# Performance work log

Hardware: AMD Instinct MI355X
Metric: run time of the kernel (lower is better)

## Reference

```python
import jax, jax.numpy as jnp
import numpy as np

N_NODES = 2000
N_EDGES = 8000  # undirected; 2*N_EDGES directed pairs
BATCH = 16
D = 64  # in/out node and edge feature dim


def _build_graph():
    """Random undirected graph; returns directed (src, dst) pairs in the
    row-major order of torch.where(adj==1), plus the undirected edge id of
    each directed pair (mimics get_all_edge_for_node_pairs)."""
    rng = np.random.default_rng(0)
    cand = rng.integers(0, N_NODES, size=(6 * N_EDGES, 2))
    cand = cand[cand[:, 0] != cand[:, 1]]
    cand = np.sort(cand, axis=1)
    cand = np.unique(cand, axis=0)
    und = cand[:N_EDGES]  # [E,2] unique undirected edges
    adj = np.zeros((N_NODES, N_NODES), dtype=np.int64)
    eid = np.full((N_NODES, N_NODES), -1, dtype=np.int64)
    e = np.arange(N_EDGES)
    adj[und[:, 0], und[:, 1]] = 1
    adj[und[:, 1], und[:, 0]] = 1
    eid[und[:, 0], und[:, 1]] = e
    eid[und[:, 1], und[:, 0]] = e
    src, dst = np.nonzero(adj)  # row-major, like torch.where
    edge_idx = eid[src, dst]
    return src.astype(np.int32), dst.astype(np.int32), edge_idx.astype(np.int32)


def setup_inputs() -> dict:
    key = jax.random.key(0)
    ks = jax.random.split(key, 7)
    src, dst, eidx = _build_graph()
    s = 0.05
    return {
        "x": jax.random.normal(ks[0], (BATCH, N_EDGES + N_NODES, D), jnp.float32),
        "W_edge": jax.random.normal(ks[1], (D, D), jnp.float32) * s,
        "W_node": jax.random.normal(ks[2], (D, D), jnp.float32) * s,
        "b_node": jax.random.normal(ks[3], (D,), jnp.float32) * s,
        "W_comb": jax.random.normal(ks[4], (3 * D, D), jnp.float32) * s,
        "b_comb": jax.random.normal(ks[5], (D,), jnp.float32) * s,
        "w_attn": jax.random.normal(ks[6], (D, 1), jnp.float32) * s,
        "src": jnp.asarray(src),
        "dst": jnp.asarray(dst),
        "eidx": jnp.asarray(eidx),
        "num_edges": N_EDGES,
    }


def reference(x, W_edge, W_node, b_node, W_comb, b_comb, w_attn, src, dst, eidx, num_edges):
    E = num_edges
    edges = x[:, :E]            # [B,E,D]
    nodes = x[:, E:]            # [B,N,D]
    B, N = nodes.shape[0], nodes.shape[1]
    f = edges @ W_edge          # dense_edge (no bias)      [B,E,D]
    h = nodes @ W_node + b_node  # dense_node (bias)        [B,N,D]
    # gather per directed edge: src node, edge feat, dst node -> [B,2E,3D]
    g = jnp.concatenate([h[:, src], f[:, eidx], h[:, dst]], axis=-1)
    f_out = jax.nn.leaky_relu(g @ W_comb + b_comb, negative_slope=0.01)  # [B,2E,D]
    # attention logits -> softmax over ALL directed edges (dim=1, as in torch)
    alpha = jax.nn.softmax(jnp.einsum('bed,do->beo', f_out, w_attn), axis=1)[..., 0]  # [B,2E]
    # scatter into dense per-batch adjacency, then aggregate
    adj = jnp.zeros((B, N, N), x.dtype).at[:, src, dst].set(alpha)
    h_out = jnp.einsum('bnm,bmd->bnd', adj, h)  # [B,N,D]
    return jnp.concatenate([f_out, h_out], axis=1)  # [B,2E+N,D]
```

## Files before the change

### kernel.cpp

```cpp
#include <hip/hip_runtime.h>
#include <hip/hip_bf16.h>

#define B_ 16
#define N_ 2000
#define E_ 8000
#define P_ 16000
#define XROW (E_ + N_)
#define OROW (P_ + N_)

typedef __hip_bfloat16 bf16;
typedef unsigned short u16;
typedef unsigned int u32;
typedef __attribute__((ext_vector_type(8))) short short8;
typedef __attribute__((ext_vector_type(4))) float f32x4;

__device__ __forceinline__ float b2f(bf16 v) { return __bfloat162float(v); }
__device__ __forceinline__ float u2f(u16 u) { return __uint_as_float(((u32)u) << 16); }
__device__ __forceinline__ float lo2f(u32 u) { return __uint_as_float(u << 16); }
__device__ __forceinline__ float hi2f(u32 u) { return __uint_as_float(u & 0xFFFF0000u); }
__device__ __forceinline__ u16 f2bu(float v) {
  bf16 b = __float2bfloat16(v);
  return *reinterpret_cast<u16*>(&b);
}

__device__ __forceinline__ float ldin(const void* p, int i, int f32) {
  return f32 ? ((const float*)p)[i] : __bfloat162float(((const bf16*)p)[i]);
}

__device__ __forceinline__ int detect_f32(const void* x) {
  int lane = threadIdx.x & 63;
  ushort4 v = reinterpret_cast<const ushort4*>(x)[lane];
  int bad = 0;
  float f0 = u2f(v.x), f1 = u2f(v.y), f2 = u2f(v.z), f3 = u2f(v.w);
  if (!(fabsf(f0) < 1e4f)) bad++;
  if (!(fabsf(f1) < 1e4f)) bad++;
  if (!(fabsf(f2) < 1e4f)) bad++;
  if (!(fabsf(f3) < 1e4f)) bad++;
  unsigned long long m = __ballot(bad > 0);
  return __popcll(m) > 8;
}

__device__ __forceinline__ ushort4 ld4b(const void* p, size_t i, int f32) {
  ushort4 o;
  if (f32) {
    float4 v = *reinterpret_cast<const float4*>((const float*)p + i);
    o.x = f2bu(v.x); o.y = f2bu(v.y); o.z = f2bu(v.z); o.w = f2bu(v.w);
  } else {
    o = *reinterpret_cast<const ushort4*>((const u16*)p + i);
  }
  return o;
}

__global__ __launch_bounds__(256) void k_pre(
    const void* __restrict__ x,
    const void* __restrict__ W_edge, const void* __restrict__ W_node,
    const void* __restrict__ b_node, const void* __restrict__ W_comb,
    float* __restrict__ A1, float* __restrict__ A2, float* __restrict__ A3,
    float* __restrict__ c1, float* __restrict__ c3) {
  const int f32 = detect_f32(x);
  int o = blockIdx.x * 256 + threadIdx.x;
  if (o < 4096) {
    int i = o >> 6, j = o & 63;
    float a = 0.f;
    for (int k = 0; k < 64; ++k) a += ldin(W_node, i*64+k, f32) * ldin(W_comb, k*64+j, f32);
    A1[o] = a;
  } else if (o < 8192) {
    int oo = o - 4096; int i = oo >> 6, j = oo & 63;
    float a = 0.f;
    for (int k = 0; k < 64; ++k) a += ldin(W_edge, i*64+k, f32) * ldin(W_comb, (64+k)*64+j, f32);
    A2[oo] = a;
  } else if (o < 12288) {
    int oo = o - 8192; int i = oo >> 6, j = oo & 63;
    float a = 0.f;
    for (int k = 0; k < 64; ++k) a += ldin(W_node, i*64+k, f32) * ldin(W_comb, (128+k)*64+j, f32);
    A3[oo] = a;
  } else if (o < 12352) {
    int j = o - 12288;
    float a = 0.f;
    for (int k = 0; k < 64; ++k) a += ldin(b_node, k, f32) * ldin(W_comb, k*64+j, f32);
    c1[j] = a;
  } else if (o < 12416) {
    int j = o - 12352;
    float a = 0.f;
    for (int k = 0; k < 64; ++k) a += ldin(b_node, k, f32) * ldin(W_comb, (128+k)*64+j, f32);
    c3[j] = a;
  }
}

#define PITCH 72
__global__ __launch_bounds__(256) void k_transform(
    const void* __restrict__ x, const void* __restrict__ W_node,
    const void* __restrict__ b_node,
    const float* __restrict__ A1, const float* __restrict__ A2,
    const float* __restrict__ A3,
    const float* __restrict__ c1, const float* __restrict__ c3,
    bf16* __restrict__ h, bf16* __restrict__ hs, bf16* __restrict__ hd,
    bf16* __restrict__ fe) {
  __shared__ u16 smem[128*PITCH + 64*PITCH < 256*PITCH ? 256*PITCH : 256*PITCH];
  const int f32 = detect_f32(x);
  int t = threadIdx.x;
  int wave = t >> 6, lane = t & 63;
  int m16 = lane & 15, q = lane >> 4;
  if (blockIdx.x < 500) {
    u16* xs = smem;
    u16* Wt = smem + 64*PITCH;
    int row0 = blockIdx.x * 64;
    for (int i = t*4; i < 4096; i += 1024) {
      int r = i >> 6, k = i & 63;
      int row = row0 + r;
      int b = row / N_, n = row - b * N_;
      *reinterpret_cast<ushort4*>(&xs[r*PITCH + k]) =
          ld4b(x, (size_t)(b * XROW + E_ + n) * 64 + k, f32);
    }
    for (int idx = t; idx < 192*16; idx += 256) {
      int c = idx >> 4, kg = (idx & 15) * 4;
      ushort4 o;
      u16* ov = (u16*)&o;
      #pragma unroll
      for (int j = 0; j < 4; ++j) {
        int k = kg + j;
        float v;
        if (c < 64)        v = ldin(W_node, k*64 + c, f32);
        else if (c < 128)  v = A1[k*64 + (c - 64)];
        else               v = A3[k*64 + (c - 128)];
        ov[j] = f2bu(v);
      }
      *reinterpret_cast<ushort4*>(&Wt[c*PITCH + kg]) = o;
    }
    __syncthreads();
    int mrow = wave*16 + m16;
    short8 af0 = *reinterpret_cast<short8*>(&xs[mrow*PITCH + q*8]);
    short8 af1 = *reinterpret_cast<short8*>(&xs[mrow*PITCH + 32 + q*8]);
    f32x4 acc[12];
    #pragma unroll
    for (int c = 0; c < 12; ++c) acc[c] = (f32x4){0.f, 0.f, 0.f, 0.f};
    #pragma unroll
    for (int c = 0; c < 12; ++c) {
      short8 bf0 = *reinterpret_cast<short8*>(&Wt[(c*16 + m16)*PITCH + q*8]);
      short8 bf1 = *reinterpret_cast<short8*>(&Wt[(c*16 + m16)*PITCH + 32 + q*8]);
      acc[c] = __builtin_amdgcn_mfma_f32_16x16x32_bf16(af0, bf0, acc[c], 0, 0, 0);
      acc[c] = __builtin_amdgcn_mfma_f32_16x16x32_bf16(af1, bf1, acc[c], 0, 0, 0);
    }
    #pragma unroll
    for (int c = 0; c < 12; ++c) {
      int seg = c >> 2;
      int lcol = (c*16 + m16) & 63;
      float bias = (seg == 0) ? ldin(b_node, lcol, f32) : (seg == 1 ? c1[lcol] : c3[lcol]);
      bf16* tgt = (seg == 0) ? h : (seg == 1 ? hs : hd);
      #pragma unroll
      for (int r = 0; r < 4; ++r) {
        int row = row0 + wave*16 + q*4 + r;
        tgt[(size_t)row*64 + lcol] = __float2bfloat16(acc[c][r] + bias);
      }
    }
  } else {
    u16* xs = smem;
    u16* Wt = smem + 128*PITCH;
    int row0 = (blockIdx.x - 500) * 128;
    for (int i = t*4; i < 8192; i += 1024) {
      int r = i >> 6, k = i & 63;
      int row = row0 + r;
      int b = row / E_, e = row - b * E_;
      *reinterpret_cast<ushort4*>(&xs[r*PITCH + k]) =
          ld4b(x, (size_t)(b * XROW + e) * 64 + k, f32);
    }
    for (int idx = t; idx < 64*16; idx += 256) {
      int c = idx >> 4, kg = (idx & 15) * 4;
      ushort4 o;
      u16* ov = (u16*)&o;
      #pragma unroll
      for (int j = 0; j < 4; ++j) ov[j] = f2bu(A2[(kg + j)*64 + c]);
      *reinterpret_cast<ushort4*>(&Wt[c*PITCH + kg]) = o;
    }
    __syncthreads();
    short8 af[2][2];
    #pragma unroll
    for (int rt = 0; rt < 2; ++rt) {
      int mrow = wave*32 + rt*16 + m16;
      af[rt][0] = *reinterpret_cast<short8*>(&xs[mrow*PITCH + q*8]);
      af[rt][1] = *reinterpret_cast<short8*>(&xs[mrow*PITCH + 32 + q*8]);
    }
    f32x4 acc[2][4];
    #pragma unroll
    for (int rt = 0; rt < 2; ++rt)
      #pragma unroll
      for (int c = 0; c < 4; ++c) acc[rt][c] = (f32x4){0.f, 0.f, 0.f, 0.f};
    #pragma unroll
    for (int c = 0; c < 4; ++c) {
      short8 bf0 = *reinterpret_cast<short8*>(&Wt[(c*16 + m16)*PITCH + q*8]);
      short8 bf1 = *reinterpret_cast<short8*>(&Wt[(c*16 + m16)*PITCH + 32 + q*8]);
      #pragma unroll
      for (int rt = 0; rt < 2; ++rt) {
        acc[rt][c] = __builtin_amdgcn_mfma_f32_16x16x32_bf16(af[rt][0], bf0, acc[rt][c], 0, 0, 0);
        acc[rt][c] = __builtin_amdgcn_mfma_f32_16x16x32_bf16(af[rt][1], bf1, acc[rt][c], 0, 0, 0);
      }
    }
    #pragma unroll
    for (int rt = 0; rt < 2; ++rt)
      #pragma unroll
      for (int c = 0; c < 4; ++c) {
        int col = c*16 + m16;
        #pragma unroll
        for (int r = 0; r < 4; ++r) {
          int row = row0 + wave*32 + rt*16 + q*4 + r;
          fe[(size_t)row*64 + col] = __float2bfloat16(acc[rt][c][r]);
        }
      }
  }
}

__global__ __launch_bounds__(256) void k_combine(
    const void* __restrict__ x,
    const bf16* __restrict__ hs, const bf16* __restrict__ hd,
    const bf16* __restrict__ fe, const void* __restrict__ b_comb,
    const void* __restrict__ w_attn,
    const int* __restrict__ src, const int* __restrict__ dst,
    const int* __restrict__ eidx,
    void* __restrict__ out, float* __restrict__ logits,
    float* __restrict__ mpart, float* __restrict__ spart) {
  const int f32 = detect_f32(x);
  __shared__ float bias[64], watt[64];
  __shared__ float ld_log[32];
  int t = threadIdx.x;
  if (t < 64) { bias[t] = ldin(b_comb, t, f32); watt[t] = ldin(w_attn, t, f32); }
  __syncthreads();
  int lane = t & 63, wave = t >> 6;
  int grp = lane >> 3, sub = lane & 7, c0 = sub * 8;
  int r = blockIdx.x * 32 + wave * 8 + grp;
  int b = r / P_, p = r - b * P_;
  int s = src[p], d2 = dst[p], e = eidx[p];
  uint4 ua = *reinterpret_cast<const uint4*>((const u16*)hs + (size_t)(b*N_ + s)*64 + c0);
  uint4 uf = *reinterpret_cast<const uint4*>((const u16*)fe + (size_t)(b*E_ + e)*64 + c0);
  uint4 ud = *reinterpret_cast<const uint4*>((const u16*)hd + (size_t)(b*N_ + d2)*64 + c0);
  float v[8];
  v[0] = lo2f(ua.x) + lo2f(uf.x) + lo2f(ud.x) + bias[c0+0];
  v[1] = hi2f(ua.x) + hi2f(uf.x) + hi2f(ud.x) + bias[c0+1];
  v[2] = lo2f(ua.y) + lo2f(uf.y) + lo2f(ud.y) + bias[c0+2];
  v[3] = hi2f(ua.y) + hi2f(uf.y) + hi2f(ud.y) + bias[c0+3];
  v[4] = lo2f(ua.z) + lo2f(uf.z) + lo2f(ud.z) + bias[c0+4];
  v[5] = hi2f(ua.z) + hi2f(uf.z) + hi2f(ud.z) + bias[c0+5];
  v[6] = lo2f(ua.w) + lo2f(uf.w) + lo2f(ud.w) + bias[c0+6];
  v[7] = hi2f(ua.w) + hi2f(uf.w) + hi2f(ud.w) + bias[c0+7];
  float l = 0.f;
  #pragma unroll
  for (int j = 0; j < 8; ++j) {
    v[j] = v[j] > 0.f ? v[j] : 0.01f * v[j];
    l += v[j] * watt[c0 + j];
  }
  size_t obase = (size_t)(b*OROW + p)*64 + c0;
  if (f32) {
    float4 o0; o0.x = v[0]; o0.y = v[1]; o0.z = v[2]; o0.w = v[3];
    float4 o1; o1.x = v[4]; o1.y = v[5]; o1.z = v[6]; o1.w = v[7];
    *reinterpret_cast<float4*>((float*)out + obase)     = o0;
    *reinterpret_cast<float4*>((float*)out + obase + 4) = o1;
  } else {
    uint4 o;
    o.x = ((u32)f2bu(v[1]) << 16) | f2bu(v[0]);
    o.y = ((u32)f2bu(v[3]) << 16) | f2bu(v[2]);
    o.z = ((u32)f2bu(v[5]) << 16) | f2bu(v[4]);
    o.w = ((u32)f2bu(v[7]) << 16) | f2bu(v[6]);
    *reinterpret_cast<uint4*>((u16*)out + obase) = o;
  }
  l += __shfl_down(l, 4, 8);
  l += __shfl_down(l, 2, 8);
  l += __shfl_down(l, 1, 8);
  if (sub == 0) {
    logits[b*P_ + p] = l;
    ld_log[wave * 8 + grp] = l;
  }
  __syncthreads();
  if (t < 32) {
    float li = ld_log[t];
    float m = li;
    #pragma unroll
    for (int o = 16; o > 0; o >>= 1) m = fmaxf(m, __shfl_xor(m, o, 32));
    float sv = __expf(li - m);
    #pragma unroll
    for (int o = 16; o > 0; o >>= 1) sv += __shfl_xor(sv, o, 32);
    if (t == 0) { mpart[blockIdx.x] = m; spart[blockIdx.x] = sv; }
  }
}

__global__ __launch_bounds__(256) void k_hout(
    const void* __restrict__ x,
    const bf16* __restrict__ h, const float* __restrict__ logits,
    const float* __restrict__ mpart, const float* __restrict__ spart,
    const int* __restrict__ src, const int* __restrict__ dst,
    void* __restrict__ out) {
  const int f32 = detect_f32(x);
  int n = blockIdx.x;
  int t = threadIdx.x;
  int wave = t >> 6, lane = t & 63;
  int b = blockIdx.y * 4 + wave;
  float m = -1e30f, s = 0.f;
  for (int j = lane; j < 500; j += 64) {
    float mj = mpart[500*b + j], sj = spart[500*b + j];
    float nm = fmaxf(m, mj);
    s = s * __expf(m - nm) + sj * __expf(mj - nm);
    m = nm;
  }
  #pragma unroll
  for (int o = 32; o > 0; o >>= 1) {
    float mo = __shfl_xor(m, o, 64);
    float so = __shfl_xor(s, o, 64);
    float nm = fmaxf(m, mo);
    s = s * __expf(m - nm) + so * __expf(mo - nm);
    m = nm;
  }
  float inv = 1.0f / s;
  int lo = 0, hi = P_;
  while (lo < hi) { int mid = (lo + hi) >> 1; if (src[mid] < n) lo = mid + 1; else hi = mid; }
  int start = lo;
  hi = P_;
  while (lo < hi) { int mid = (lo + hi) >> 1; if (src[mid] <= n) lo = mid + 1; else hi = mid; }
  int end = lo;
  int grp = lane >> 4, sub = lane & 15, c0 = sub * 4;
  float a0 = 0.f, a1 = 0.f, a2 = 0.f, a3 = 0.f;
  for (int p = start + grp; p < end; p += 4) {
    float a = __expf(logits[b*P_ + p] - m) * inv;
    int dn = dst[p];
    ushort4 hv = *reinterpret_cast<const ushort4*>((const u16*)h + (size_t)(b*N_ + dn)*64 + c0);
    a0 += a * u2f(hv.x); a1 += a * u2f(hv.y);
    a2 += a * u2f(hv.z); a3 += a * u2f(hv.w);
  }
  a0 += __shfl_xor(a0, 16, 64); a0 += __shfl_xor(a0, 32, 64);
  a1 += __shfl_xor(a1, 16, 64); a1 += __shfl_xor(a1, 32, 64);
  a2 += __shfl_xor(a2, 16, 64); a2 += __shfl_xor(a2, 32, 64);
  a3 += __shfl_xor(a3, 16, 64); a3 += __shfl_xor(a3, 32, 64);
  if (grp == 0) {
    size_t obase = (size_t)(b*OROW + P_ + n)*64 + c0;
    if (f32) {
      float4 o4; o4.x = a0; o4.y = a1; o4.z = a2; o4.w = a3;
      *reinterpret_cast<float4*>((float*)out + obase) = o4;
    } else {
      ushort4 o4;
      o4.x = f2bu(a0); o4.y = f2bu(a1); o4.z = f2bu(a2); o4.w = f2bu(a3);
      *reinterpret_cast<ushort4*>((u16*)out + obase) = o4;
    }
  }
}

extern "C" void kernel_launch(void* const* d_in, const int* in_sizes, int n_in,
                              void* d_out, int out_size, void* d_ws, size_t ws_size,
                              hipStream_t stream) {
  const void* x      = d_in[0];
  const void* W_edge = d_in[1];
  const void* W_node = d_in[2];
  const void* b_node = d_in[3];
  const void* W_comb = d_in[4];
  const void* b_comb = d_in[5];
  const void* w_attn = d_in[6];
  const int* src  = (const int*)d_in[7];
  const int* dst  = (const int*)d_in[8];
  const int* eidx = (const int*)d_in[9];

  float* A1 = (float*)d_ws;
  float* A2 = A1 + 4096;
  float* A3 = A2 + 4096;
  float* c1 = A3 + 4096;
  float* c3 = c1 + 64;
  float* logits = c3 + 64;
  float* mpart = logits + B_*P_;
  float* spart = mpart + 8000;
  bf16* h  = (bf16*)(spart + 8000);
  bf16* hs = h  + B_*N_*64;
  bf16* hd = hs + B_*N_*64;
  bf16* fe = hd + B_*N_*64;

  k_pre<<<49, 256, 0, stream>>>(x, W_edge, W_node, b_node, W_comb, A1, A2, A3, c1, c3);
  k_transform<<<1500, 256, 0, stream>>>(x, W_node, b_node, A1, A2, A3, c1, c3, h, hs, hd, fe);
  k_combine<<<(B_*P_)/32, 256, 0, stream>>>(x, hs, hd, fe, b_comb, w_attn, src, dst, eidx, d_out, logits, mpart, spart);
  k_hout<<<dim3(N_, B_/4), 256, 0, stream>>>(x, h, logits, mpart, spart, src, dst, d_out);
}
```

Measured before the change: 196.4 us.

## Precompute bf16 transposed weights, CSR rowptr, and softmax stats in separate kernels

k_pre now writes the transposed bf16 combined weight matrices and a CSR row pointer for src, so k_transform no longer rebuilds weight tiles in shared memory per block. k_transform loads MFMA operands straight from global memory without LDS staging. A new k_smerge kernel merges the per-block softmax max/sum once per batch, and k_hout reads those values plus rowptr instead of redoing the reduction and binary searches in every block. This adds one kernel launch and relies on uncoalesced global fragment loads in the transform.

```diff
diff --git a/kernel.cpp b/kernel.cpp
--- a/kernel.cpp
+++ b/kernel.cpp
@@ -40,106 +40,95 @@
   return __popcll(m) > 8;
 }
 
-__device__ __forceinline__ ushort4 ld4b(const void* p, size_t i, int f32) {
-  ushort4 o;
+__device__ __forceinline__ short8 ld8b(const void* p, size_t i, int f32) {
+  short8 r;
   if (f32) {
-    float4 v = *reinterpret_cast<const float4*>((const float*)p + i);
-    o.x = f2bu(v.x); o.y = f2bu(v.y); o.z = f2bu(v.z); o.w = f2bu(v.w);
+    const float* f = (const float*)p + i;
+    float4 v0 = *reinterpret_cast<const float4*>(f);
+    float4 v1 = *reinterpret_cast<const float4*>(f + 4);
+    u16* o = (u16*)&r;
+    o[0] = f2bu(v0.x); o[1] = f2bu(v0.y); o[2] = f2bu(v0.z); o[3] = f2bu(v0.w);
+    o[4] = f2bu(v1.x); o[5] = f2bu(v1.y); o[6] = f2bu(v1.z); o[7] = f2bu(v1.w);
   } else {
-    o = *reinterpret_cast<const ushort4*>((const u16*)p + i);
-  }
-  return o;
+    r = *reinterpret_cast<const short8*>((const u16*)p + i);
+  }
+  return r;
 }
 
 __global__ __launch_bounds__(256) void k_pre(
     const void* __restrict__ x,
     const void* __restrict__ W_edge, const void* __restrict__ W_node,
     const void* __restrict__ b_node, const void* __restrict__ W_comb,
-    float* __restrict__ A1, float* __restrict__ A2, float* __restrict__ A3,
-    float* __restrict__ c1, float* __restrict__ c3) {
+    const int* __restrict__ src,
+    u16* __restrict__ Wtn, u16* __restrict__ Wte,
+    float* __restrict__ c1, float* __restrict__ c3,
+    int* __restrict__ rowptr) {
   const int f32 = detect_f32(x);
   int o = blockIdx.x * 256 + threadIdx.x;
   if (o < 4096) {
-    int i = o >> 6, j = o & 63;
+    int c = o >> 6, k = o & 63;
+    Wtn[c*64 + k] = f2bu(ldin(W_node, k*64 + c, f32));
+  } else if (o < 12288) {
+    int oo = o - 4096;
+    int cc = oo >> 6, k = oo & 63;
+    int col = cc & 63;
+    int base = (cc < 64) ? 0 : 128;
     float a = 0.f;
-    for (int k = 0; k < 64; ++k) a += ldin(W_node, i*64+k, f32) * ldin(W_comb, k*64+j, f32);
-    A1[o] = a;
-  } else if (o < 8192) {
-    int oo = o - 4096; int i = oo >> 6, j = oo & 63;
+    for (int j = 0; j < 64; ++j)
+      a += ldin(W_node, k*64 + j, f32) * ldin(W_comb, (base + j)*64 + col, f32);
+    Wtn[(64 + cc)*64 + k] = f2bu(a);
+  } else if (o < 16384) {
+    int oo = o - 12288;
+    int c = oo >> 6, k = oo & 63;
     float a = 0.f;
-    for (int k = 0; k < 64; ++k) a += ldin(W_edge, i*64+k, f32) * ldin(W_comb, (64+k)*64+j, f32);
-    A2[oo] = a;
-  } else if (o < 12288) {
-    int oo = o - 8192; int i = oo >> 6, j = oo & 63;
+    for (int j = 0; j < 64; ++j)
+      a += ldin(W_edge, k*64 + j, f32) * ldin(W_comb, (64 + j)*64 + c, f32);
+    Wte[c*64 + k] = f2bu(a);
+  } else if (o < 16448) {
+    int j = o - 16384;
     float a = 0.f;
-    for (int k = 0; k < 64; ++k) a += ldin(W_node, i*64+k, f32) * ldin(W_comb, (128+k)*64+j, f32);
-    A3[oo] = a;
-  } else if (o < 12352) {
-    int j = o - 12288;
+    for (int k = 0; k < 64; ++k) a += ldin(b_node, k, f32) * ldin(W_comb, k*64 + j, f32);
+    c1[j] = a;
+  } else if (o < 16512) {
+    int j = o - 16448;
     float a = 0.f;
-    for (int k = 0; k < 64; ++k) a += ldin(b_node, k, f32) * ldin(W_comb, k*64+j, f32);
-    c1[j] = a;
-  } else if (o < 12416) {
-    int j = o - 12352;
-    float a = 0.f;
-    for (int k = 0; k < 64; ++k) a += ldin(b_node, k, f32) * ldin(W_comb, (128+k)*64+j, f32);
+    for (int k = 0; k < 64; ++k) a += ldin(b_node, k, f32) * ldin(W_comb, (128 + k)*64 + j, f32);
     c3[j] = a;
-  }
-}
-
-#define PITCH 72
+  } else if (o < 16512 + N_ + 1) {
+    int n = o - 16512;
+    int lo = 0, hi = P_;
+    while (lo < hi) { int mid = (lo + hi) >> 1; if (src[mid] < n) lo = mid + 1; else hi = mid; }
+    rowptr[n] = lo;
+  }
+}
+
 __global__ __launch_bounds__(256) void k_transform(
-    const void* __restrict__ x, const void* __restrict__ W_node,
+    const void* __restrict__ x,
+    const u16* __restrict__ Wtn, const u16* __restrict__ Wte,
     const void* __restrict__ b_node,
-    const float* __restrict__ A1, const float* __restrict__ A2,
-    const float* __restrict__ A3,
     const float* __restrict__ c1, const float* __restrict__ c3,
     bf16* __restrict__ h, bf16* __restrict__ hs, bf16* __restrict__ hd,
     bf16* __restrict__ fe) {
-  __shared__ u16 smem[128*PITCH + 64*PITCH < 256*PITCH ? 256*PITCH : 256*PITCH];
   const int f32 = detect_f32(x);
   int t = threadIdx.x;
   int wave = t >> 6, lane = t & 63;
   int m16 = lane & 15, q = lane >> 4;
   if (blockIdx.x < 500) {
-    u16* xs = smem;
-    u16* Wt = smem + 64*PITCH;
-    int row0 = blockIdx.x * 64;
-    for (int i = t*4; i < 4096; i += 1024) {
-      int r = i >> 6, k = i & 63;
-      int row = row0 + r;
-      int b = row / N_, n = row - b * N_;
-      *reinterpret_cast<ushort4*>(&xs[r*PITCH + k]) =
-          ld4b(x, (size_t)(b * XROW + E_ + n) * 64 + k, f32);
-    }
-    for (int idx = t; idx < 192*16; idx += 256) {
-      int c = idx >> 4, kg = (idx & 15) * 4;
-      ushort4 o;
-      u16* ov = (u16*)&o;
-      #pragma unroll
-      for (int j = 0; j < 4; ++j) {
-        int k = kg + j;
-        float v;
-        if (c < 64)        v = ldin(W_node, k*64 + c, f32);
-        else if (c < 128)  v = A1[k*64 + (c - 64)];
-        else               v = A3[k*64 + (c - 128)];
-        ov[j] = f2bu(v);
-      }
-      *reinterpret_cast<ushort4*>(&Wt[c*PITCH + kg]) = o;
-    }
-    __syncthreads();
-    int mrow = wave*16 + m16;
-    short8 af0 = *reinterpret_cast<short8*>(&xs[mrow*PITCH + q*8]);
-    short8 af1 = *reinterpret_cast<short8*>(&xs[mrow*PITCH + 32 + q*8]);
+    int row0 = blockIdx.x * 64 + wave * 16;
+    int arow = row0 + m16;
+    int b = arow / N_, n = arow - b * N_;
+    size_t xbase = (size_t)(b * XROW + E_ + n) * 64;
+    short8 af0 = ld8b(x, xbase + q*8, f32);
+    short8 af1 = ld8b(x, xbase + 32 + q*8, f32);
     f32x4 acc[12];
     #pragma unroll
     for (int c = 0; c < 12; ++c) acc[c] = (f32x4){0.f, 0.f, 0.f, 0.f};
     #pragma unroll
     for (int c = 0; c < 12; ++c) {
-      short8 bf0 = *reinterpret_cast<short8*>(&Wt[(c*16 + m16)*PITCH + q*8]);
-      short8 bf1 = *reinterpret_cast<short8*>(&Wt[(c*16 + m16)*PITCH + 32 + q*8]);
-      acc[c] = __builtin_amdgcn_mfma_f32_16x16x32_bf16(af0, bf0, acc[c], 0, 0, 0);
-      acc[c] = __builtin_amdgcn_mfma_f32_16x16x32_bf16(af1, bf1, acc[c], 0, 0, 0);
+      short8 b0 = *reinterpret_cast<const short8*>(&Wtn[(c*16 + m16)*64 + q*8]);
+      short8 b1 = *reinterpret_cast<const short8*>(&Wtn[(c*16 + m16)*64 + 32 + q*8]);
+      acc[c] = __builtin_amdgcn_mfma_f32_16x16x32_bf16(af0, b0, acc[c], 0, 0, 0);
+      acc[c] = __builtin_amdgcn_mfma_f32_16x16x32_bf16(af1, b1, acc[c], 0, 0, 0);
     }
     #pragma unroll
     for (int c = 0; c < 12; ++c) {
@@ -149,36 +138,20 @@
       bf16* tgt = (seg == 0) ? h : (seg == 1 ? hs : hd);
       #pragma unroll
       for (int r = 0; r < 4; ++r) {
-        int row = row0 + wave*16 + q*4 + r;
+        int row = row0 + q*4 + r;
         tgt[(size_t)row*64 + lcol] = __float2bfloat16(acc[c][r] + bias);
       }
     }
   } else {
-    u16* xs = smem;
-    u16* Wt = smem + 128*PITCH;
-    int row0 = (blockIdx.x - 500) * 128;
-    for (int i = t*4; i < 8192; i += 1024) {
-      int r = i >> 6, k = i & 63;
-      int row = row0 + r;
-      int b = row / E_, e = row - b * E_;
-      *reinterpret_cast<ushort4*>(&xs[r*PITCH + k]) =
-          ld4b(x, (size_t)(b * XROW + e) * 64 + k, f32);
-    }
-    for (int idx = t; idx < 64*16; idx += 256) {
-      int c = idx >> 4, kg = (idx & 15) * 4;
-      ushort4 o;
-      u16* ov = (u16*)&o;
-      #pragma unroll
-      for (int j = 0; j < 4; ++j) ov[j] = f2bu(A2[(kg + j)*64 + c]);
-      *reinterpret_cast<ushort4*>(&Wt[c*PITCH + kg]) = o;
-    }
-    __syncthreads();
+    int row0 = (blockIdx.x - 500) * 128 + wave * 32;
     short8 af[2][2];
     #pragma unroll
     for (int rt = 0; rt < 2; ++rt) {
-      int mrow = wave*32 + rt*16 + m16;
-      af[rt][0] = *reinterpret_cast<short8*>(&xs[mrow*PITCH + q*8]);
-      af[rt][1] = *reinterpret_cast<short8*>(&xs[mrow*PITCH + 32 + q*8]);
+      int arow = row0 + rt*16 + m16;
+      int b = arow / E_, e = arow - b * E_;
+      size_t xbase = (size_t)(b * XROW + e) * 64;
+      af[rt][0] = ld8b(x, xbase + q*8, f32);
+      af[rt][1] = ld8b(x, xbase + 32 + q*8, f32);
     }
     f32x4 acc[2][4];
     #pragma unroll
@@ -187,12 +160,12 @@
       for (int c = 0; c < 4; ++c) acc[rt][c] = (f32x4){0.f, 0.f, 0.f, 0.f};
     #pragma unroll
     for (int c = 0; c < 4; ++c) {
-      short8 bf0 = *reinterpret_cast<short8*>(&Wt[(c*16 + m16)*PITCH + q*8]);
-      short8 bf1 = *reinterpret_cast<short8*>(&Wt[(c*16 + m16)*PITCH + 32 + q*8]);
+      short8 b0 = *reinterpret_cast<const short8*>(&Wte[(c*16 + m16)*64 + q*8]);
+      short8 b1 = *reinterpret_cast<const short8*>(&Wte[(c*16 + m16)*64 + 32 + q*8]);
       #pragma unroll
       for (int rt = 0; rt < 2; ++rt) {
-        acc[rt][c] = __builtin_amdgcn_mfma_f32_16x16x32_bf16(af[rt][0], bf0, acc[rt][c], 0, 0, 0);
-        acc[rt][c] = __builtin_amdgcn_mfma_f32_16x16x32_bf16(af[rt][1], bf1, acc[rt][c], 0, 0, 0);
+        acc[rt][c] = __builtin_amdgcn_mfma_f32_16x16x32_bf16(af[rt][0], b0, acc[rt][c], 0, 0, 0);
+        acc[rt][c] = __builtin_amdgcn_mfma_f32_16x16x32_bf16(af[rt][1], b1, acc[rt][c], 0, 0, 0);
       }
     }
     #pragma unroll
@@ -202,7 +175,7 @@
         int col = c*16 + m16;
         #pragma unroll
         for (int r = 0; r < 4; ++r) {
-          int row = row0 + wave*32 + rt*16 + q*4 + r;
+          int row = row0 + rt*16 + q*4 + r;
           fe[(size_t)row*64 + col] = __float2bfloat16(acc[rt][c][r]);
         }
       }
@@ -281,39 +254,44 @@
   }
 }
 
+__global__ __launch_bounds__(256) void k_smerge(
+    const float* __restrict__ mpart, const float* __restrict__ spart,
+    float* __restrict__ mb, float* __restrict__ sb) {
+  __shared__ float rm[256], rs[256];
+  int b = blockIdx.x, t = threadIdx.x;
+  float m = -1e30f, s = 0.f;
+  for (int j = t; j < 500; j += 256) {
+    float mj = mpart[500*b + j], sj = spart[500*b + j];
+    float nm = fmaxf(m, mj);
+    s = s * __expf(m - nm) + sj * __expf(mj - nm);
+    m = nm;
+  }
+  rm[t] = m; rs[t] = s; __syncthreads();
+  for (int st = 128; st > 0; st >>= 1) {
+    if (t < st) {
+      float mo = rm[t + st], so = rs[t + st];
+      float nm = fmaxf(rm[t], mo);
+      rs[t] = rs[t] * __expf(rm[t] - nm) + so * __expf(mo - nm);
+      rm[t] = nm;
+    }
+    __syncthreads();
+  }
+  if (t == 0) { mb[b] = rm[0]; sb[b] = 1.0f / rs[0]; }
+}
+
 __global__ __launch_bounds__(256) void k_hout(
     const void* __restrict__ x,
     const bf16* __restrict__ h, const float* __restrict__ logits,
-    const float* __restrict__ mpart, const float* __restrict__ spart,
-    const int* __restrict__ src, const int* __restrict__ dst,
+    const float* __restrict__ mb, const float* __restrict__ sb,
+    const int* __restrict__ rowptr, const int* __restrict__ dst,
     void* __restrict__ out) {
   const int f32 = detect_f32(x);
   int n = blockIdx.x;
   int t = threadIdx.x;
   int wave = t >> 6, lane = t & 63;
   int b = blockIdx.y * 4 + wave;
-  float m = -1e30f, s = 0.f;
-  for (int j = lane; j < 500; j += 64) {
-    float mj = mpart[500*b + j], sj = spart[500*b + j];
-    float nm = fmaxf(m, mj);
-    s = s * __expf(m - nm) + sj * __expf(mj - nm);
-    m = nm;
-  }
-  #pragma unroll
-  for (int o = 32; o > 0; o >>= 1) {
-    float mo = __shfl_xor(m, o, 64);
-    float so = __shfl_xor(s, o, 64);
-    float nm = fmaxf(m, mo);
-    s = s * __expf(m - nm) + so * __expf(mo - nm);
-    m = nm;
-  }
-  float inv = 1.0f / s;
-  int lo = 0, hi = P_;
-  while (lo < hi) { int mid = (lo + hi) >> 1; if (src[mid] < n) lo = mid + 1; else hi = mid; }
-  int start = lo;
-  hi = P_;
-  while (lo < hi) { int mid = (lo + hi) >> 1; if (src[mid] <= n) lo = mid + 1; else hi = mid; }
-  int end = lo;
+  float m = mb[b], inv = sb[b];
+  int start = rowptr[n], end = rowptr[n + 1];
   int grp = lane >> 4, sub = lane & 15, c0 = sub * 4;
   float a0 = 0.f, a1 = 0.f, a2 = 0.f, a3 = 0.f;
   for (int p = start + grp; p < end; p += 4) {
@@ -354,21 +332,24 @@
   const int* dst  = (const int*)d_in[8];
   const int* eidx = (const int*)d_in[9];
 
-  float* A1 = (float*)d_ws;
-  float* A2 = A1 + 4096;
-  float* A3 = A2 + 4096;
-  float* c1 = A3 + 4096;
-  float* c3 = c1 + 64;
-  float* logits = c3 + 64;
-  float* mpart = logits + B_*P_;
-  float* spart = mpart + 8000;
-  bf16* h  = (bf16*)(spart + 8000);
-  bf16* hs = h  + B_*N_*64;
-  bf16* hd = hs + B_*N_*64;
-  bf16* fe = hd + B_*N_*64;
-
-  k_pre<<<49, 256, 0, stream>>>(x, W_edge, W_node, b_node, W_comb, A1, A2, A3, c1, c3);
-  k_transform<<<1500, 256, 0, stream>>>(x, W_node, b_node, A1, A2, A3, c1, c3, h, hs, hd, fe);
+  float* logits = (float*)d_ws;
+  float* mpart  = logits + B_*P_;
+  float* spart  = mpart + 8000;
+  float* mb     = spart + 8000;
+  float* sb     = mb + B_;
+  float* c1     = sb + B_;
+  float* c3     = c1 + 64;
+  int*   rowptr = (int*)(c3 + 64);
+  u16*   Wtn    = (u16*)(rowptr + 2016);
+  u16*   Wte    = Wtn + 192*64;
+  bf16*  h      = (bf16*)(Wte + 64*64);
+  bf16*  hs     = h  + B_*N_*64;
+  bf16*  hd     = hs + B_*N_*64;
+  bf16*  fe     = hd + B_*N_*64;
+
+  k_pre<<<73, 256, 0, stream>>>(x, W_edge, W_node, b_node, W_comb, src, Wtn, Wte, c1, c3, rowptr);
+  k_transform<<<1500, 256, 0, stream>>>(x, Wtn, Wte, b_node, c1, c3, h, hs, hd, fe);
   k_combine<<<(B_*P_)/32, 256, 0, stream>>>(x, hs, hd, fe, b_comb, w_attn, src, dst, eidx, d_out, logits, mpart, spart);
-  k_hout<<<dim3(N_, B_/4), 256, 0, stream>>>(x, h, logits, mpart, spart, src, dst, d_out);
-}
+  k_smerge<<<B_, 256, 0, stream>>>(mpart, spart, mb, sb);
+  k_hout<<<dim3(N_, B_/4), 256, 0, stream>>>(x, h, logits, mb, sb, rowptr, dst, d_out);
+}
```

Result: faster. 179.8 us (-8.4%).
